# Kernel tuning notes

Measured on AMD Instinct MI355X. Metric: run time of the kernel, lower is better.

## Reference

```python
import jax, jax.numpy as jnp
import numpy as np

B, N, C = 32, 2048, 64  # graphs, points per graph, hidden channels


def _linear_params(key, fin, fout):
    k1, k2 = jax.random.split(key)
    bound = 1.0 / np.sqrt(fin)
    W = jax.random.uniform(k1, (fin, fout), minval=-bound, maxval=bound, dtype=jnp.float32)
    b = jax.random.uniform(k2, (fout,), minval=-bound, maxval=bound, dtype=jnp.float32)
    return W, b


def setup_inputs() -> dict:
    key = jax.random.key(0)
    ks = jax.random.split(key, 10)
    W1a, b1a = _linear_params(ks[0], 3 * 2 + 3, C)   # conv1 mlp layer 1 (h is pos, 3-dim)
    W1b, b1b = _linear_params(ks[1], C, C)
    W2a, b2a = _linear_params(ks[2], C * 2 + 3, C)   # conv2
    W2b, b2b = _linear_params(ks[3], C, C)
    W3a, b3a = _linear_params(ks[4], C * 2 + 3, C)   # conv3
    W3b, b3b = _linear_params(ks[5], C, C)
    Wr, br = _linear_params(ks[6], C, 6)
    pos = jax.random.normal(ks[7], (B * N, 3), dtype=jnp.float32)
    x = jax.random.normal(ks[8], (B * N, 3), dtype=jnp.float32)  # unused by forward (h=pos)
    batch = jnp.repeat(jnp.arange(B, dtype=jnp.int32), N)
    return dict(x=x, pos=pos, batch=batch,
                W1a=W1a, b1a=b1a, W1b=W1b, b1b=b1b,
                W2a=W2a, b2a=b2a, W2b=W2b, b2b=b2b,
                W3a=W3a, b3a=b3a, W3b=W3b, b3b=b3b,
                Wr=Wr, br=br)


_gather = jax.vmap(lambda a, i: a[i])  # per-graph fancy gather


def knn_idx(pos, k):
    # pos: [B, n, 3] -> idx [B, n, k] of k nearest neighbors (incl. self, loop=True)
    d2 = jnp.sum((pos[:, :, None, :] - pos[:, None, :, :]) ** 2, axis=-1)  # [B,n,n]
    _, idx = jax.lax.top_k(-d2, k)
    return idx


def fps_idx(pos_b, m):
    # farthest point sampling of m points from pos_b [n,3], deterministic start at 0
    d = jnp.sum((pos_b - pos_b[0]) ** 2, axis=-1)
    def body(d, _):
        i = jnp.argmax(d)
        d = jnp.minimum(d, jnp.sum((pos_b - pos_b[i]) ** 2, axis=-1))
        return d, i
    _, rest = jax.lax.scan(body, d, None, length=m - 1)
    return jnp.concatenate([jnp.zeros((1,), rest.dtype), rest])


def pointnet_layer(h, pos, idx, W1, b1, W2, b2):
    # h [B,n,Ch], pos [B,n,3], idx [B,n,k]; message = mlp(cat(h_i,h_j,pos_j-pos_i)); aggr = max
    h_j = _gather(h, idx)                      # [B,n,k,Ch]
    pos_j = _gather(pos, idx)                  # [B,n,k,3]
    rel = pos_j - pos[:, :, None, :]
    h_i = jnp.broadcast_to(h[:, :, None, :], h_j.shape)
    m = jnp.concatenate([h_i, h_j, rel], axis=-1)
    m = jax.nn.relu(m @ W1 + b1) @ W2 + b2
    return jnp.max(m, axis=2)                  # max over neighbors -> [B,n,C]


def reference(x, pos, batch,
              W1a, b1a, W1b, b1b,
              W2a, b2a, W2b, b2b,
              W3a, b3a, W3b, b3b,
              Wr, br):
    p = pos.reshape(B, N, 3)
    # layer 1: h = pos, k = 6
    h = jax.nn.relu(pointnet_layer(p, p, knn_idx(p, 6), W1a, b1a, W1b, b1b))
    # fps ratio 0.5 -> N/2
    sel = jax.vmap(lambda pb: fps_idx(pb, N // 2))(p)
    p, h = _gather(p, sel), _gather(h, sel)
    # layer 2: k = 4
    h = jax.nn.relu(pointnet_layer(h, p, knn_idx(p, 4), W2a, b2a, W2b, b2b))
    # fps -> N/4
    sel = jax.vmap(lambda pb: fps_idx(pb, N // 4))(p)
    p, h = _gather(p, sel), _gather(h, sel)
    # layer 3: k = 3
    h = jax.nn.relu(pointnet_layer(h, p, knn_idx(p, 3), W3a, b3a, W3b, b3b))
    g = jnp.max(h, axis=1)  # global max pool over points -> [B, C]
    return g @ Wr + br      # [B, 6]
```

## Files before the change

### kernel.cpp

```cpp
#include <hip/hip_runtime.h>
#include <hip/hip_bf16.h>
#include <math.h>

constexpr int B = 32;
constexpr int N = 2048;

__global__ void detect_kernel(const unsigned int* __restrict__ raw, int* __restrict__ flag) {
    __shared__ int cnt;
    if (threadIdx.x == 0) cnt = 0;
    __syncthreads();
    int c = 0;
    for (int i = threadIdx.x; i < 4096; i += 256) {
        unsigned h = (raw[i] >> 8) & 0x7f;
        if (h >= 0x3a && h <= 0x41) c++;
    }
    atomicAdd(&cnt, c);
    __syncthreads();
    if (threadIdx.x == 0) *flag = (cnt > (4096 * 55) / 100) ? 1 : 0;
}

__global__ void b2f_kernel(const void* __restrict__ in, float* __restrict__ out, int n,
                           const int* __restrict__ flag) {
    int i = blockIdx.x * 256 + threadIdx.x;
    if (i >= n) return;
    if (*flag) out[i] = __bfloat162float(((const __hip_bfloat16*)in)[i]);
    else       out[i] = ((const float*)in)[i];
}

struct B2FMulti {
    const void* src[14];
    float* dst[14];
    int n[14];
};

__global__ void b2f_multi_kernel(B2FMulti p, const int* __restrict__ flag) {
    int a = blockIdx.y;
    int i = blockIdx.x * 256 + threadIdx.x;
    if (i >= p.n[a]) return;
    if (*flag) p.dst[a][i] = __bfloat162float(((const __hip_bfloat16*)p.src[a])[i]);
    else       p.dst[a][i] = ((const float*)p.src[a])[i];
}

template <int K>
__global__ void __launch_bounds__(256) knn_kernel(const float* __restrict__ pos,
                                                  int* __restrict__ idx_out, int n) {
    #pragma clang fp contract(off)
    const int b = blockIdx.y;
    const int i = blockIdx.x * 256 + threadIdx.x;
    const float* pb = pos + (size_t)b * n * 3;
    const float xi = pb[i * 3 + 0], yi = pb[i * 3 + 1], zi = pb[i * 3 + 2];

    float bd[K];
    int   bi_[K];
    #pragma unroll
    for (int q = 0; q < K; ++q) { bd[q] = __builtin_inff(); bi_[q] = 0x7fffffff; }

    __shared__ float tx[256], ty[256], tz[256];
    for (int t0 = 0; t0 < n; t0 += 256) {
        __syncthreads();
        {
            int j = t0 + threadIdx.x;
            tx[threadIdx.x] = pb[j * 3 + 0];
            ty[threadIdx.x] = pb[j * 3 + 1];
            tz[threadIdx.x] = pb[j * 3 + 2];
        }
        __syncthreads();
        for (int jj = 0; jj < 256; ++jj) {
            float dx = xi - tx[jj], dy = yi - ty[jj], dz = zi - tz[jj];
            float d2 = (dx * dx + dy * dy) + dz * dz;
            int jg = t0 + jj;
            if (d2 < bd[K - 1] || (d2 == bd[K - 1] && jg < bi_[K - 1])) {
                bd[K - 1] = d2; bi_[K - 1] = jg;
                #pragma unroll
                for (int q = K - 1; q > 0; --q) {
                    bool sw = (bd[q] < bd[q - 1]) || (bd[q] == bd[q - 1] && bi_[q] < bi_[q - 1]);
                    if (sw) {
                        float td = bd[q]; bd[q] = bd[q - 1]; bd[q - 1] = td;
                        int   ti = bi_[q]; bi_[q] = bi_[q - 1]; bi_[q - 1] = ti;
                    }
                }
            }
        }
    }
    int* op = idx_out + ((size_t)b * n + i) * K;
    #pragma unroll
    for (int q = 0; q < K; ++q) op[q] = bi_[q];
}

template <int NPTS>
__device__ __forceinline__ void fps_phase(const float* __restrict__ px,
                                          const float* __restrict__ py,
                                          const float* __restrict__ pz,
                                          int* __restrict__ sel_lds,
                                          unsigned long long* __restrict__ slots,
                                          int m, int t) {
    #pragma clang fp contract(off)
    constexpr int P = NPTS / 256;
    float d[P], ox[P], oy[P], oz[P];
    unsigned int nk[P];
    const float sx = px[0], sy = py[0], sz = pz[0];
    #pragma unroll
    for (int p = 0; p < P; ++p) {
        const int ii = t * P + p;
        ox[p] = px[ii]; oy[p] = py[ii]; oz[p] = pz[ii];
        float dx = ox[p] - sx, dy = oy[p] - sy, dz = oz[p] - sz;
        d[p] = (dx * dx + dy * dy) + dz * dz;
        nk[p] = ~(unsigned)ii;
    }
    if (t == 0) sel_lds[0] = 0;

    for (int it = 1; it < m; ++it) {
        unsigned long long kb = ((unsigned long long)__float_as_uint(d[0]) << 32) | nk[0];
        #pragma unroll
        for (int p = 1; p < P; ++p) {
            unsigned long long key = ((unsigned long long)__float_as_uint(d[p]) << 32) | nk[p];
            if (key > kb) kb = key;
        }
        #pragma unroll
        for (int o = 1; o < 64; o <<= 1) {
            unsigned long long other = __shfl_xor(kb, o, 64);
            if (other > kb) kb = other;
        }
        if ((t & 63) == 0) slots[(it & 1) * 4 + (t >> 6)] = kb;
        __syncthreads();
        {
            const unsigned long long* sp = slots + (it & 1) * 4;
            unsigned long long k0 = sp[0], k1 = sp[1], k2 = sp[2], k3 = sp[3];
            if (k1 > k0) k0 = k1;
            if (k3 > k2) k2 = k3;
            kb = (k2 > k0) ? k2 : k0;
        }
        const int bix = (int)(~(unsigned)(kb & 0xffffffffULL));
        if (t == 0) sel_lds[it] = bix;
        const float nx = px[bix], ny = py[bix], nz = pz[bix];
        #pragma unroll
        for (int p = 0; p < P; ++p) {
            float dx = ox[p] - nx, dy = oy[p] - ny, dz = oz[p] - nz;
            float dd = (dx * dx + dy * dy) + dz * dz;
            d[p] = fminf(d[p], dd);
        }
    }
    __syncthreads();
}

__global__ void __launch_bounds__(256) mega_kernel(
        const float* __restrict__ posf, const int* __restrict__ idx1,
        const float* __restrict__ W1, const float* __restrict__ b1,
        const float* __restrict__ W2, const float* __restrict__ b2,
        float* __restrict__ h1, int* __restrict__ sel1, int* __restrict__ sel2,
        float* __restrict__ p2, float* __restrict__ p3) {
    __shared__ __align__(16) char smem[65536];
    const int t = threadIdx.x;

    if (blockIdx.x < B) {
        const int b = blockIdx.x;
        float* px = (float*)smem;
        float* py = px + 2048;
        float* pz = py + 2048;
        int*   sel1_l = (int*)(pz + 2048);
        float* qx = (float*)(sel1_l + 1024);
        float* qy = qx + 1024;
        float* qz = qy + 1024;
        int*   sel2_l = (int*)(qz + 1024);
        unsigned long long* slots = (unsigned long long*)(sel2_l + 512);

        const float* pb = posf + (size_t)b * N * 3;
        for (int i = t; i < N; i += 256) {
            px[i] = pb[i * 3 + 0]; py[i] = pb[i * 3 + 1]; pz[i] = pb[i * 3 + 2];
        }
        __syncthreads();

        fps_phase<2048>(px, py, pz, sel1_l, slots, 1024, t);

        for (int i = t; i < 1024; i += 256) {
            int s = sel1_l[i];
            qx[i] = px[s]; qy[i] = py[s]; qz[i] = pz[s];
            sel1[(size_t)b * 1024 + i] = s;
        }
        __syncthreads();
        for (int i = t; i < 1024; i += 256) {
            float* pp = p2 + ((size_t)b * 1024 + i) * 3;
            pp[0] = qx[i]; pp[1] = qy[i]; pp[2] = qz[i];
        }

        fps_phase<1024>(qx, qy, qz, sel2_l, slots, 512, t);

        for (int i = t; i < 512; i += 256) {
            int s = sel2_l[i];
            sel2[(size_t)b * 512 + i] = s;
            float* pp = p3 + ((size_t)b * 512 + i) * 3;
            pp[0] = qx[s]; pp[1] = qy[s]; pp[2] = qz[s];
        }
    } else {
        const int lane = t & 63, g = t >> 6;
        float* al = (float*)smem + g * 4096;
        const int flat = (blockIdx.x - B) * 256 + t;
        const int b = flat >> 11;
        const int i = flat & (N - 1);
        const float* pb = posf + (size_t)b * N * 3;
        const float xi = pb[i * 3 + 0], yi = pb[i * 3 + 1], zi = pb[i * 3 + 2];

        float acc[64];
        #pragma unroll
        for (int c = 0; c < 64; ++c) acc[c] = -__builtin_inff();

        const int* idxp = idx1 + (size_t)flat * 6;
        for (int kk = 0; kk < 6; ++kk) {
            const int j = idxp[kk];
            const float xj = pb[j * 3 + 0], yj = pb[j * 3 + 1], zj = pb[j * 3 + 2];
            const float mv[9] = {xi, yi, zi, xj, yj, zj, xj - xi, yj - yi, zj - zi};
            float a[64];
            #pragma unroll
            for (int e = 0; e < 64; ++e) a[e] = b1[e];
            #pragma unroll
            for (int d = 0; d < 9; ++d) {
                #pragma unroll
                for (int e = 0; e < 64; ++e) a[e] = fmaf(mv[d], W1[d * 64 + e], a[e]);
            }
            __syncthreads();
            #pragma unroll
            for (int e = 0; e < 64; ++e) al[e * 64 + lane] = fmaxf(a[e], 0.f);
            __syncthreads();
            float o[64];
            #pragma unroll
            for (int c = 0; c < 64; ++c) o[c] = b2[c];
            for (int e = 0; e < 64; ++e) {
                float av = al[e * 64 + lane];
                #pragma unroll
                for (int c = 0; c < 64; ++c) o[c] = fmaf(av, W2[e * 64 + c], o[c]);
            }
            #pragma unroll
            for (int c = 0; c < 64; ++c) acc[c] = fmaxf(acc[c], o[c]);
        }
        float* op = h1 + (size_t)flat * 64;
        #pragma unroll
        for (int c = 0; c < 64; ++c) op[c] = fmaxf(acc[c], 0.f);
    }
}

__global__ void gather_h_kernel(const float* __restrict__ h_in, const int* __restrict__ sel,
                                float* __restrict__ h_out, int n_in, int m) {
    const int b = blockIdx.y;
    const int tid = blockIdx.x * 256 + threadIdx.x;
    const int p = tid >> 6, c = tid & 63;
    if (p >= m) return;
    const int s = sel[(size_t)b * m + p];
    h_out[((size_t)b * m + p) * 64 + c] = h_in[((size_t)b * n_in + s) * 64 + c];
}

__global__ void __launch_bounds__(64) pointnet64_kernel(
        const float* __restrict__ h_in, const float* __restrict__ pos,
        const int* __restrict__ idx,
        const float* __restrict__ W1, const float* __restrict__ b1,
        const float* __restrict__ W2, const float* __restrict__ b2,
        float* __restrict__ out, int n, int k) {
    const int b = blockIdx.y, lane = threadIdx.x;
    const int i = blockIdx.x * 64 + lane;
    const float* pb = pos + (size_t)b * n * 3;
    const float* hb = h_in + (size_t)b * n * 64;
    const float xi = pb[i * 3 + 0], yi = pb[i * 3 + 1], zi = pb[i * 3 + 2];

    __shared__ float a_lds[64 * 64];

    float acc[64];
    #pragma unroll
    for (int c = 0; c < 64; ++c) acc[c] = -__builtin_inff();

    const int* idxp = idx + ((size_t)b * n + i) * k;
    const float* hi = hb + (size_t)i * 64;
    for (int kk = 0; kk < k; ++kk) {
        const int j = idxp[kk];
        const float xj = pb[j * 3 + 0], yj = pb[j * 3 + 1], zj = pb[j * 3 + 2];
        const float* hj = hb + (size_t)j * 64;

        float a[64];
        #pragma unroll
        for (int e = 0; e < 64; ++e) a[e] = b1[e];

        for (int d4 = 0; d4 < 16; ++d4) {
            float4 v = *(const float4*)(hi + d4 * 4);
            const float mu[4] = {v.x, v.y, v.z, v.w};
            const float* wr = W1 + (size_t)(d4 * 4) * 64;
            #pragma unroll
            for (int u = 0; u < 4; ++u) {
                #pragma unroll
                for (int e = 0; e < 64; ++e) a[e] = fmaf(mu[u], wr[u * 64 + e], a[e]);
            }
        }
        for (int d4 = 0; d4 < 16; ++d4) {
            float4 v = *(const float4*)(hj + d4 * 4);
            const float mu[4] = {v.x, v.y, v.z, v.w};
            const float* wr = W1 + (size_t)(64 + d4 * 4) * 64;
            #pragma unroll
            for (int u = 0; u < 4; ++u) {
                #pragma unroll
                for (int e = 0; e < 64; ++e) a[e] = fmaf(mu[u], wr[u * 64 + e], a[e]);
            }
        }
        {
            const float mr[3] = {xj - xi, yj - yi, zj - zi};
            #pragma unroll
            for (int d = 0; d < 3; ++d) {
                #pragma unroll
                for (int e = 0; e < 64; ++e) a[e] = fmaf(mr[d], W1[(128 + d) * 64 + e], a[e]);
            }
        }
        __syncthreads();
        #pragma unroll
        for (int e = 0; e < 64; ++e) a_lds[e * 64 + lane] = fmaxf(a[e], 0.f);
        __syncthreads();
        float o[64];
        #pragma unroll
        for (int c = 0; c < 64; ++c) o[c] = b2[c];
        for (int e = 0; e < 64; ++e) {
            float av = a_lds[e * 64 + lane];
            #pragma unroll
            for (int c = 0; c < 64; ++c) o[c] = fmaf(av, W2[e * 64 + c], o[c]);
        }
        #pragma unroll
        for (int c = 0; c < 64; ++c) acc[c] = fmaxf(acc[c], o[c]);
    }
    float* op = out + ((size_t)b * n + i) * 64;
    #pragma unroll
    for (int c = 0; c < 64; ++c) op[c] = fmaxf(acc[c], 0.f);
}

__global__ void __launch_bounds__(64) head_kernel(const float* __restrict__ h,
                                                  const float* __restrict__ Wr,
                                                  const float* __restrict__ br,
                                                  void* __restrict__ out, int n,
                                                  const int* __restrict__ flag) {
    const int b = blockIdx.x, lane = threadIdx.x;
    const float* hb = h + (size_t)b * n * 64;
    float g = -__builtin_inff();
    for (int i = 0; i < n; ++i) g = fmaxf(g, hb[(size_t)i * 64 + lane]);
    __shared__ float gl[64];
    gl[lane] = g;
    __syncthreads();
    if (lane < 6) {
        float o = br[lane];
        #pragma unroll
        for (int c = 0; c < 64; ++c) o = fmaf(gl[c], Wr[c * 6 + lane], o);
        if (*flag) ((__hip_bfloat16*)out)[b * 6 + lane] = __float2bfloat16(o);
        else       ((float*)out)[b * 6 + lane] = o;
    }
}

extern "C" void kernel_launch(void* const* d_in, const int* in_sizes, int n_in,
                              void* d_out, int out_size, void* d_ws, size_t ws_size,
                              hipStream_t stream) {
    (void)in_sizes; (void)n_in; (void)out_size; (void)ws_size;

    char* w = (char*)d_ws;
    auto alloc = [&](size_t nbytes) -> void* {
        void* p = (void*)w;
        w += (nbytes + 255) & ~(size_t)255;
        return p;
    };

    int*   flag = (int*)alloc(4);
    float* posf = (float*)alloc((size_t)B * N * 3 * 4);
    float* W1a = (float*)alloc(9 * 64 * 4);    float* b1a = (float*)alloc(64 * 4);
    float* W1b = (float*)alloc(64 * 64 * 4);   float* b1b = (float*)alloc(64 * 4);
    float* W2a = (float*)alloc(131 * 64 * 4);  float* b2a = (float*)alloc(64 * 4);
    float* W2b = (float*)alloc(64 * 64 * 4);   float* b2b = (float*)alloc(64 * 4);
    float* W3a = (float*)alloc(131 * 64 * 4);  float* b3a = (float*)alloc(64 * 4);
    float* W3b = (float*)alloc(64 * 64 * 4);   float* b3b = (float*)alloc(64 * 4);
    float* Wr  = (float*)alloc(64 * 6 * 4);    float* br  = (float*)alloc(6 * 4);

    float* h1    = (float*)alloc((size_t)B * N * 64 * 4);
    int*   idx1  = (int*)alloc((size_t)B * N * 6 * 4);
    int*   sel1  = (int*)alloc((size_t)B * 1024 * 4);
    float* p2    = (float*)alloc((size_t)B * 1024 * 3 * 4);
    float* h2in  = (float*)alloc((size_t)B * 1024 * 64 * 4);
    int*   idx2  = (int*)alloc((size_t)B * 1024 * 4 * 4);
    int*   sel2  = (int*)alloc((size_t)B * 512 * 4);
    float* p3    = (float*)alloc((size_t)B * 512 * 3 * 4);
    int*   idx3  = (int*)alloc((size_t)B * 512 * 3 * 4);
    float* h2out = h1;
    float* h3in  = h1 + (size_t)B * 1024 * 64;
    float* h3out = h1 + (size_t)B * 1024 * 64 + (size_t)B * 512 * 64;

    detect_kernel<<<dim3(1), 256, 0, stream>>>((const unsigned int*)d_in[1], flag);
    b2f_kernel<<<dim3((B * N * 3 + 255) / 256), 256, 0, stream>>>(d_in[1], posf, B * N * 3, flag);
    B2FMulti mp;
    {
        const int   wi[14] = {3, 4, 5, 6, 7, 8, 9, 10, 11, 12, 13, 14, 15, 16};
        float*      wd[14] = {W1a, b1a, W1b, b1b, W2a, b2a, W2b, b2b, W3a, b3a, W3b, b3b, Wr, br};
        const int   wn[14] = {576, 64, 4096, 64, 8384, 64, 4096, 64, 8384, 64, 4096, 64, 384, 6};
        for (int q = 0; q < 14; ++q) { mp.src[q] = d_in[wi[q]]; mp.dst[q] = wd[q]; mp.n[q] = wn[q]; }
    }
    b2f_multi_kernel<<<dim3(33, 14), 256, 0, stream>>>(mp, flag);

    knn_kernel<6><<<dim3(N / 256, B), 256, 0, stream>>>(posf, idx1, N);

    mega_kernel<<<dim3(B + (B * N) / 256), 256, 0, stream>>>(posf, idx1, W1a, b1a, W1b, b1b,
                                                             h1, sel1, sel2, p2, p3);

    gather_h_kernel<<<dim3(1024 * 64 / 256, B), 256, 0, stream>>>(h1, sel1, h2in, N, 1024);
    knn_kernel<4><<<dim3(1024 / 256, B), 256, 0, stream>>>(p2, idx2, 1024);
    pointnet64_kernel<<<dim3(1024 / 64, B), 64, 0, stream>>>(h2in, p2, idx2, W2a, b2a, W2b, b2b,
                                                             h2out, 1024, 4);

    gather_h_kernel<<<dim3(512 * 64 / 256, B), 256, 0, stream>>>(h2out, sel2, h3in, 1024, 512);
    knn_kernel<3><<<dim3(512 / 256, B), 256, 0, stream>>>(p3, idx3, 512);
    pointnet64_kernel<<<dim3(512 / 64, B), 64, 0, stream>>>(h3in, p3, idx3, W3a, b3a, W3b, b3b,
                                                            h3out, 512, 3);

    head_kernel<<<dim3(B), 64, 0, stream>>>(h3out, Wr, br, d_out, 512, flag);
}
```

Baseline: 2.276 ms.

## Fuse knn, gather and head into layer kernels; use DPP float argmax in FPS

Merges the two conversion kernels into one launch. The knn search now runs inside each layer kernel with the point coordinates staged in LDS, and the FPS gathers are folded into the layer-2 and layer-3 loads. The global max pool and regression head move into the layer-3 kernel using LDS atomics. FPS replaces the 64-bit shuffle argmax with a float DPP max, a ballot and a readlane. The kernels also drop the LDS-staged second MLP in favour of an all-register two-half loop. The aim is fewer launches and less intermediate global traffic. The cost is much higher register pressure, and layer 3 now runs on only 32 blocks of 512 threads, which lowers parallelism.

```diff
diff --git a/kernel.cpp b/kernel.cpp
--- a/kernel.cpp
+++ b/kernel.cpp
@@ -19,73 +19,20 @@
     if (threadIdx.x == 0) *flag = (cnt > (4096 * 55) / 100) ? 1 : 0;
 }
 
-__global__ void b2f_kernel(const void* __restrict__ in, float* __restrict__ out, int n,
-                           const int* __restrict__ flag) {
+struct ConvSeg { const void* src; float* dst; int n; };
+struct ConvParams { ConvSeg s[15]; };
+
+__global__ void convert_kernel(ConvParams p, const int* __restrict__ flag) {
+    const ConvSeg sg = p.s[blockIdx.y];
     int i = blockIdx.x * 256 + threadIdx.x;
-    if (i >= n) return;
-    if (*flag) out[i] = __bfloat162float(((const __hip_bfloat16*)in)[i]);
-    else       out[i] = ((const float*)in)[i];
-}
-
-struct B2FMulti {
-    const void* src[14];
-    float* dst[14];
-    int n[14];
-};
-
-__global__ void b2f_multi_kernel(B2FMulti p, const int* __restrict__ flag) {
-    int a = blockIdx.y;
-    int i = blockIdx.x * 256 + threadIdx.x;
-    if (i >= p.n[a]) return;
-    if (*flag) p.dst[a][i] = __bfloat162float(((const __hip_bfloat16*)p.src[a])[i]);
-    else       p.dst[a][i] = ((const float*)p.src[a])[i];
-}
-
-template <int K>
-__global__ void __launch_bounds__(256) knn_kernel(const float* __restrict__ pos,
-                                                  int* __restrict__ idx_out, int n) {
-    #pragma clang fp contract(off)
-    const int b = blockIdx.y;
-    const int i = blockIdx.x * 256 + threadIdx.x;
-    const float* pb = pos + (size_t)b * n * 3;
-    const float xi = pb[i * 3 + 0], yi = pb[i * 3 + 1], zi = pb[i * 3 + 2];
-
-    float bd[K];
-    int   bi_[K];
-    #pragma unroll
-    for (int q = 0; q < K; ++q) { bd[q] = __builtin_inff(); bi_[q] = 0x7fffffff; }
-
-    __shared__ float tx[256], ty[256], tz[256];
-    for (int t0 = 0; t0 < n; t0 += 256) {
-        __syncthreads();
-        {
-            int j = t0 + threadIdx.x;
-            tx[threadIdx.x] = pb[j * 3 + 0];
-            ty[threadIdx.x] = pb[j * 3 + 1];
-            tz[threadIdx.x] = pb[j * 3 + 2];
-        }
-        __syncthreads();
-        for (int jj = 0; jj < 256; ++jj) {
-            float dx = xi - tx[jj], dy = yi - ty[jj], dz = zi - tz[jj];
-            float d2 = (dx * dx + dy * dy) + dz * dz;
-            int jg = t0 + jj;
-            if (d2 < bd[K - 1] || (d2 == bd[K - 1] && jg < bi_[K - 1])) {
-                bd[K - 1] = d2; bi_[K - 1] = jg;
-                #pragma unroll
-                for (int q = K - 1; q > 0; --q) {
-                    bool sw = (bd[q] < bd[q - 1]) || (bd[q] == bd[q - 1] && bi_[q] < bi_[q - 1]);
-                    if (sw) {
-                        float td = bd[q]; bd[q] = bd[q - 1]; bd[q - 1] = td;
-                        int   ti = bi_[q]; bi_[q] = bi_[q - 1]; bi_[q - 1] = ti;
-                    }
-                }
-            }
-        }
-    }
-    int* op = idx_out + ((size_t)b * n + i) * K;
-    #pragma unroll
-    for (int q = 0; q < K; ++q) op[q] = bi_[q];
-}
+    if (i >= sg.n) return;
+    if (*flag) sg.dst[i] = __bfloat162float(((const __hip_bfloat16*)sg.src)[i]);
+    else       sg.dst[i] = ((const float*)sg.src)[i];
+}
+
+#define DPP_MAXF(v, ctrl)                                                      \
+    (v) = fmaxf((v), __int_as_float(__builtin_amdgcn_update_dpp(               \
+        __float_as_int(v), __float_as_int(v), (ctrl), 0xf, 0xf, false)))
 
 template <int NPTS>
 __device__ __forceinline__ void fps_phase(const float* __restrict__ px,
@@ -97,62 +44,145 @@
     #pragma clang fp contract(off)
     constexpr int P = NPTS / 256;
     float d[P], ox[P], oy[P], oz[P];
-    unsigned int nk[P];
-    const float sx = px[0], sy = py[0], sz = pz[0];
     #pragma unroll
     for (int p = 0; p < P; ++p) {
         const int ii = t * P + p;
         ox[p] = px[ii]; oy[p] = py[ii]; oz[p] = pz[ii];
-        float dx = ox[p] - sx, dy = oy[p] - sy, dz = oz[p] - sz;
-        d[p] = (dx * dx + dy * dy) + dz * dz;
-        nk[p] = ~(unsigned)ii;
+        d[p] = __builtin_inff();
     }
     if (t == 0) sel_lds[0] = 0;
+    float nx = px[0], ny = py[0], nz = pz[0];
 
     for (int it = 1; it < m; ++it) {
-        unsigned long long kb = ((unsigned long long)__float_as_uint(d[0]) << 32) | nk[0];
-        #pragma unroll
-        for (int p = 1; p < P; ++p) {
-            unsigned long long key = ((unsigned long long)__float_as_uint(d[p]) << 32) | nk[p];
-            if (key > kb) kb = key;
-        }
-        #pragma unroll
-        for (int o = 1; o < 64; o <<= 1) {
-            unsigned long long other = __shfl_xor(kb, o, 64);
-            if (other > kb) kb = other;
-        }
-        if ((t & 63) == 0) slots[(it & 1) * 4 + (t >> 6)] = kb;
-        __syncthreads();
-        {
-            const unsigned long long* sp = slots + (it & 1) * 4;
-            unsigned long long k0 = sp[0], k1 = sp[1], k2 = sp[2], k3 = sp[3];
-            if (k1 > k0) k0 = k1;
-            if (k3 > k2) k2 = k3;
-            kb = (k2 > k0) ? k2 : k0;
-        }
-        const int bix = (int)(~(unsigned)(kb & 0xffffffffULL));
-        if (t == 0) sel_lds[it] = bix;
-        const float nx = px[bix], ny = py[bix], nz = pz[bix];
+        float bv = -1.0f; int bix = 0;
         #pragma unroll
         for (int p = 0; p < P; ++p) {
             float dx = ox[p] - nx, dy = oy[p] - ny, dz = oz[p] - nz;
             float dd = (dx * dx + dy * dy) + dz * dz;
-            d[p] = fminf(d[p], dd);
-        }
-    }
-    __syncthreads();
-}
-
-__global__ void __launch_bounds__(256) mega_kernel(
-        const float* __restrict__ posf, const int* __restrict__ idx1,
+            float dn = fminf(d[p], dd);
+            d[p] = dn;
+            if (dn > bv) { bv = dn; bix = t * P + p; }
+        }
+        float r = bv;
+        DPP_MAXF(r, 0x111); DPP_MAXF(r, 0x112); DPP_MAXF(r, 0x114);
+        DPP_MAXF(r, 0x118); DPP_MAXF(r, 0x142); DPP_MAXF(r, 0x143);
+        const float gmax = __int_as_float(__builtin_amdgcn_readlane(__float_as_int(r), 63));
+        const unsigned long long msk = __ballot(bv == gmax);
+        const int wl = (int)__builtin_ctzll(msk);
+        const int widx = __builtin_amdgcn_readlane(bix, wl);
+        if ((t & 63) == 0) {
+            slots[(it & 1) * 4 + (t >> 6)] =
+                ((unsigned long long)(unsigned)__float_as_int(gmax) << 32) |
+                (unsigned)(~widx);
+        }
+        __syncthreads();
+        const unsigned long long* sp = slots + (it & 1) * 4;
+        unsigned long long k0 = sp[0], k1 = sp[1], k2 = sp[2], k3 = sp[3];
+        if (k1 > k0) k0 = k1;
+        if (k3 > k2) k2 = k3;
+        if (k2 > k0) k0 = k2;
+        const int g = ~(int)(unsigned)(k0 & 0xffffffffULL);
+        if (t == 0) sel_lds[it] = g;
+        nx = px[g]; ny = py[g]; nz = pz[g];
+    }
+    __syncthreads();
+}
+
+template <int K>
+__device__ __forceinline__ void knn_lds(const float* __restrict__ cx,
+                                        const float* __restrict__ cy,
+                                        const float* __restrict__ cz,
+                                        int n, float xi, float yi, float zi,
+                                        int* __restrict__ nb_l, int t, int tstride) {
+    #pragma clang fp contract(off)
+    float bd[K]; int bi_[K];
+    #pragma unroll
+    for (int q = 0; q < K; ++q) { bd[q] = __builtin_inff(); bi_[q] = 0x7fffffff; }
+    for (int j = 0; j < n; ++j) {
+        float dx = xi - cx[j], dy = yi - cy[j], dz = zi - cz[j];
+        float d2 = (dx * dx + dy * dy) + dz * dz;
+        if (d2 < bd[K - 1] || (d2 == bd[K - 1] && j < bi_[K - 1])) {
+            bd[K - 1] = d2; bi_[K - 1] = j;
+            #pragma unroll
+            for (int q = K - 1; q > 0; --q) {
+                bool sw = (bd[q] < bd[q - 1]) || (bd[q] == bd[q - 1] && bi_[q] < bi_[q - 1]);
+                if (sw) {
+                    float td = bd[q]; bd[q] = bd[q - 1]; bd[q - 1] = td;
+                    int   ti = bi_[q]; bi_[q] = bi_[q - 1]; bi_[q - 1] = ti;
+                }
+            }
+        }
+    }
+    #pragma unroll
+    for (int q = 0; q < K; ++q) nb_l[t + tstride * q] = bi_[q];
+}
+
+__device__ __forceinline__ void mlp131_acc(const float* __restrict__ hi,
+                                           const float* __restrict__ hj,
+                                           float rx, float ry, float rz,
+                                           const float* __restrict__ W1,
+                                           const float* __restrict__ b1,
+                                           const float* __restrict__ W2,
+                                           const float* __restrict__ b2,
+                                           float acc[64]) {
+    float a[64];
+    #pragma unroll
+    for (int e = 0; e < 64; ++e) a[e] = b1[e];
+    for (int d4 = 0; d4 < 16; ++d4) {
+        float4 v = *(const float4*)(hi + d4 * 4);
+        const float mu[4] = {v.x, v.y, v.z, v.w};
+        const float* wr = W1 + (size_t)(d4 * 4) * 64;
+        #pragma unroll
+        for (int u = 0; u < 4; ++u) {
+            #pragma unroll
+            for (int e = 0; e < 64; ++e) a[e] = fmaf(mu[u], wr[u * 64 + e], a[e]);
+        }
+    }
+    for (int d4 = 0; d4 < 16; ++d4) {
+        float4 v = *(const float4*)(hj + d4 * 4);
+        const float mu[4] = {v.x, v.y, v.z, v.w};
+        const float* wr = W1 + (size_t)(64 + d4 * 4) * 64;
+        #pragma unroll
+        for (int u = 0; u < 4; ++u) {
+            #pragma unroll
+            for (int e = 0; e < 64; ++e) a[e] = fmaf(mu[u], wr[u * 64 + e], a[e]);
+        }
+    }
+    {
+        const float mr[3] = {rx, ry, rz};
+        #pragma unroll
+        for (int d = 0; d < 3; ++d) {
+            #pragma unroll
+            for (int e = 0; e < 64; ++e) a[e] = fmaf(mr[d], W1[(128 + d) * 64 + e], a[e]);
+        }
+    }
+    #pragma unroll
+    for (int h = 0; h < 2; ++h) {
+        float o[32];
+        #pragma unroll
+        for (int c = 0; c < 32; ++c) o[c] = b2[h * 32 + c];
+        #pragma unroll
+        for (int e = 0; e < 64; ++e) {
+            float av = fmaxf(a[e], 0.f);
+            #pragma unroll
+            for (int c = 0; c < 32; ++c) o[c] = fmaf(av, W2[e * 64 + h * 32 + c], o[c]);
+        }
+        #pragma unroll
+        for (int c = 0; c < 32; ++c) acc[h * 32 + c] = fmaxf(acc[h * 32 + c], o[c]);
+    }
+}
+
+__global__ void __launch_bounds__(256) front_kernel(
+        const float* __restrict__ posf,
         const float* __restrict__ W1, const float* __restrict__ b1,
         const float* __restrict__ W2, const float* __restrict__ b2,
         float* __restrict__ h1, int* __restrict__ sel1, int* __restrict__ sel2,
         float* __restrict__ p2, float* __restrict__ p3) {
-    __shared__ __align__(16) char smem[65536];
+    __shared__ __align__(16) char smem[43136];
     const int t = threadIdx.x;
 
     if (blockIdx.x < B) {
+        __builtin_amdgcn_s_setprio(1);
         const int b = blockIdx.x;
         float* px = (float*)smem;
         float* py = px + 2048;
@@ -192,22 +222,29 @@
             pp[0] = qx[s]; pp[1] = qy[s]; pp[2] = qz[s];
         }
     } else {
-        const int lane = t & 63, g = t >> 6;
-        float* al = (float*)smem + g * 4096;
-        const int flat = (blockIdx.x - B) * 256 + t;
-        const int b = flat >> 11;
-        const int i = flat & (N - 1);
+        const int f = (int)blockIdx.x - B;
+        const int b = f >> 3;
+        const int i = ((f & 7) << 8) + t;
+        float* cx = (float*)smem;
+        float* cy = cx + 2048;
+        float* cz = cy + 2048;
+        int*   nb_l = (int*)(cz + 2048);
+
         const float* pb = posf + (size_t)b * N * 3;
-        const float xi = pb[i * 3 + 0], yi = pb[i * 3 + 1], zi = pb[i * 3 + 2];
+        for (int j = t; j < N; j += 256) {
+            cx[j] = pb[j * 3 + 0]; cy[j] = pb[j * 3 + 1]; cz[j] = pb[j * 3 + 2];
+        }
+        __syncthreads();
+        const float xi = cx[i], yi = cy[i], zi = cz[i];
+        knn_lds<6>(cx, cy, cz, N, xi, yi, zi, nb_l, t, 256);
 
         float acc[64];
         #pragma unroll
         for (int c = 0; c < 64; ++c) acc[c] = -__builtin_inff();
 
-        const int* idxp = idx1 + (size_t)flat * 6;
         for (int kk = 0; kk < 6; ++kk) {
-            const int j = idxp[kk];
-            const float xj = pb[j * 3 + 0], yj = pb[j * 3 + 1], zj = pb[j * 3 + 2];
+            const int j = nb_l[t + 256 * kk];
+            const float xj = cx[j], yj = cy[j], zj = cz[j];
             const float mv[9] = {xi, yi, zi, xj, yj, zj, xj - xi, yj - yi, zj - zi};
             float a[64];
             #pragma unroll
@@ -217,132 +254,109 @@
                 #pragma unroll
                 for (int e = 0; e < 64; ++e) a[e] = fmaf(mv[d], W1[d * 64 + e], a[e]);
             }
-            __syncthreads();
-            #pragma unroll
-            for (int e = 0; e < 64; ++e) al[e * 64 + lane] = fmaxf(a[e], 0.f);
-            __syncthreads();
-            float o[64];
-            #pragma unroll
-            for (int c = 0; c < 64; ++c) o[c] = b2[c];
-            for (int e = 0; e < 64; ++e) {
-                float av = al[e * 64 + lane];
+            #pragma unroll
+            for (int h = 0; h < 2; ++h) {
+                float o[32];
                 #pragma unroll
-                for (int c = 0; c < 64; ++c) o[c] = fmaf(av, W2[e * 64 + c], o[c]);
+                for (int c = 0; c < 32; ++c) o[c] = b2[h * 32 + c];
+                #pragma unroll
+                for (int e = 0; e < 64; ++e) {
+                    float av = fmaxf(a[e], 0.f);
+                    #pragma unroll
+                    for (int c = 0; c < 32; ++c) o[c] = fmaf(av, W2[e * 64 + h * 32 + c], o[c]);
+                }
+                #pragma unroll
+                for (int c = 0; c < 32; ++c) acc[h * 32 + c] = fmaxf(acc[h * 32 + c], o[c]);
             }
-            #pragma unroll
-            for (int c = 0; c < 64; ++c) acc[c] = fmaxf(acc[c], o[c]);
-        }
-        float* op = h1 + (size_t)flat * 64;
+        }
+        float* op = h1 + ((size_t)b * N + i) * 64;
         #pragma unroll
         for (int c = 0; c < 64; ++c) op[c] = fmaxf(acc[c], 0.f);
     }
 }
 
-__global__ void gather_h_kernel(const float* __restrict__ h_in, const int* __restrict__ sel,
-                                float* __restrict__ h_out, int n_in, int m) {
-    const int b = blockIdx.y;
-    const int tid = blockIdx.x * 256 + threadIdx.x;
-    const int p = tid >> 6, c = tid & 63;
-    if (p >= m) return;
-    const int s = sel[(size_t)b * m + p];
-    h_out[((size_t)b * m + p) * 64 + c] = h_in[((size_t)b * n_in + s) * 64 + c];
-}
-
-__global__ void __launch_bounds__(64) pointnet64_kernel(
-        const float* __restrict__ h_in, const float* __restrict__ pos,
-        const int* __restrict__ idx,
+__global__ void __launch_bounds__(256) layer2_kernel(
+        const float* __restrict__ h1, const float* __restrict__ p2,
+        const int* __restrict__ sel1,
         const float* __restrict__ W1, const float* __restrict__ b1,
         const float* __restrict__ W2, const float* __restrict__ b2,
-        float* __restrict__ out, int n, int k) {
-    const int b = blockIdx.y, lane = threadIdx.x;
-    const int i = blockIdx.x * 64 + lane;
-    const float* pb = pos + (size_t)b * n * 3;
-    const float* hb = h_in + (size_t)b * n * 64;
-    const float xi = pb[i * 3 + 0], yi = pb[i * 3 + 1], zi = pb[i * 3 + 2];
-
-    __shared__ float a_lds[64 * 64];
+        float* __restrict__ h2out) {
+    __shared__ float qx[1024], qy[1024], qz[1024];
+    __shared__ int nb_l[256 * 4];
+    const int t = threadIdx.x;
+    const int b = blockIdx.x >> 2;
+    const int i = ((blockIdx.x & 3) << 8) + t;
+
+    const float* pb = p2 + (size_t)b * 1024 * 3;
+    for (int j = t; j < 1024; j += 256) {
+        qx[j] = pb[j * 3 + 0]; qy[j] = pb[j * 3 + 1]; qz[j] = pb[j * 3 + 2];
+    }
+    __syncthreads();
+    const float xi = qx[i], yi = qy[i], zi = qz[i];
+    knn_lds<4>(qx, qy, qz, 1024, xi, yi, zi, nb_l, t, 256);
+
+    const int s1i = sel1[(size_t)b * 1024 + i];
+    const float* hi = h1 + ((size_t)b * N + s1i) * 64;
 
     float acc[64];
     #pragma unroll
     for (int c = 0; c < 64; ++c) acc[c] = -__builtin_inff();
 
-    const int* idxp = idx + ((size_t)b * n + i) * k;
-    const float* hi = hb + (size_t)i * 64;
-    for (int kk = 0; kk < k; ++kk) {
-        const int j = idxp[kk];
-        const float xj = pb[j * 3 + 0], yj = pb[j * 3 + 1], zj = pb[j * 3 + 2];
-        const float* hj = hb + (size_t)j * 64;
-
-        float a[64];
-        #pragma unroll
-        for (int e = 0; e < 64; ++e) a[e] = b1[e];
-
-        for (int d4 = 0; d4 < 16; ++d4) {
-            float4 v = *(const float4*)(hi + d4 * 4);
-            const float mu[4] = {v.x, v.y, v.z, v.w};
-            const float* wr = W1 + (size_t)(d4 * 4) * 64;
-            #pragma unroll
-            for (int u = 0; u < 4; ++u) {
-                #pragma unroll
-                for (int e = 0; e < 64; ++e) a[e] = fmaf(mu[u], wr[u * 64 + e], a[e]);
-            }
-        }
-        for (int d4 = 0; d4 < 16; ++d4) {
-            float4 v = *(const float4*)(hj + d4 * 4);
-            const float mu[4] = {v.x, v.y, v.z, v.w};
-            const float* wr = W1 + (size_t)(64 + d4 * 4) * 64;
-            #pragma unroll
-            for (int u = 0; u < 4; ++u) {
-                #pragma unroll
-                for (int e = 0; e < 64; ++e) a[e] = fmaf(mu[u], wr[u * 64 + e], a[e]);
-            }
-        }
-        {
-            const float mr[3] = {xj - xi, yj - yi, zj - zi};
-            #pragma unroll
-            for (int d = 0; d < 3; ++d) {
-                #pragma unroll
-                for (int e = 0; e < 64; ++e) a[e] = fmaf(mr[d], W1[(128 + d) * 64 + e], a[e]);
-            }
-        }
-        __syncthreads();
-        #pragma unroll
-        for (int e = 0; e < 64; ++e) a_lds[e * 64 + lane] = fmaxf(a[e], 0.f);
-        __syncthreads();
-        float o[64];
-        #pragma unroll
-        for (int c = 0; c < 64; ++c) o[c] = b2[c];
-        for (int e = 0; e < 64; ++e) {
-            float av = a_lds[e * 64 + lane];
-            #pragma unroll
-            for (int c = 0; c < 64; ++c) o[c] = fmaf(av, W2[e * 64 + c], o[c]);
-        }
-        #pragma unroll
-        for (int c = 0; c < 64; ++c) acc[c] = fmaxf(acc[c], o[c]);
-    }
-    float* op = out + ((size_t)b * n + i) * 64;
+    for (int kk = 0; kk < 4; ++kk) {
+        const int j = nb_l[t + 256 * kk];
+        const int s1j = sel1[(size_t)b * 1024 + j];
+        const float* hj = h1 + ((size_t)b * N + s1j) * 64;
+        mlp131_acc(hi, hj, qx[j] - xi, qy[j] - yi, qz[j] - zi, W1, b1, W2, b2, acc);
+    }
+    float* op = h2out + ((size_t)b * 1024 + i) * 64;
     #pragma unroll
     for (int c = 0; c < 64; ++c) op[c] = fmaxf(acc[c], 0.f);
 }
 
-__global__ void __launch_bounds__(64) head_kernel(const float* __restrict__ h,
-                                                  const float* __restrict__ Wr,
-                                                  const float* __restrict__ br,
-                                                  void* __restrict__ out, int n,
-                                                  const int* __restrict__ flag) {
-    const int b = blockIdx.x, lane = threadIdx.x;
-    const float* hb = h + (size_t)b * n * 64;
-    float g = -__builtin_inff();
-    for (int i = 0; i < n; ++i) g = fmaxf(g, hb[(size_t)i * 64 + lane]);
-    __shared__ float gl[64];
-    gl[lane] = g;
-    __syncthreads();
-    if (lane < 6) {
-        float o = br[lane];
-        #pragma unroll
-        for (int c = 0; c < 64; ++c) o = fmaf(gl[c], Wr[c * 6 + lane], o);
-        if (*flag) ((__hip_bfloat16*)out)[b * 6 + lane] = __float2bfloat16(o);
-        else       ((float*)out)[b * 6 + lane] = o;
+__global__ void __launch_bounds__(512) layer3_kernel(
+        const float* __restrict__ h2, const float* __restrict__ p3,
+        const int* __restrict__ sel2,
+        const float* __restrict__ W1, const float* __restrict__ b1,
+        const float* __restrict__ W2, const float* __restrict__ b2,
+        const float* __restrict__ Wr, const float* __restrict__ br,
+        void* __restrict__ out, const int* __restrict__ flag) {
+    __shared__ float qx[512], qy[512], qz[512];
+    __shared__ int nb_l[512 * 3];
+    __shared__ int gbits[64];
+    const int t = threadIdx.x;
+    const int b = blockIdx.x;
+
+    const float* pb = p3 + (size_t)b * 512 * 3;
+    if (t < 512) { qx[t] = pb[t * 3 + 0]; qy[t] = pb[t * 3 + 1]; qz[t] = pb[t * 3 + 2]; }
+    if (t < 64) gbits[t] = 0;
+    __syncthreads();
+    const float xi = qx[t], yi = qy[t], zi = qz[t];
+    knn_lds<3>(qx, qy, qz, 512, xi, yi, zi, nb_l, t, 512);
+
+    const int s2i = sel2[(size_t)b * 512 + t];
+    const float* hi = h2 + ((size_t)b * 1024 + s2i) * 64;
+
+    float acc[64];
+    #pragma unroll
+    for (int c = 0; c < 64; ++c) acc[c] = -__builtin_inff();
+
+    for (int kk = 0; kk < 3; ++kk) {
+        const int j = nb_l[t + 512 * kk];
+        const int s2j = sel2[(size_t)b * 512 + j];
+        const float* hj = h2 + ((size_t)b * 1024 + s2j) * 64;
+        mlp131_acc(hi, hj, qx[j] - xi, qy[j] - yi, qz[j] - zi, W1, b1, W2, b2, acc);
+    }
+    #pragma unroll
+    for (int c = 0; c < 64; ++c) {
+        atomicMax(&gbits[c], __float_as_int(fmaxf(acc[c], 0.f)));
+    }
+    __syncthreads();
+    if (t < 6) {
+        float o = br[t];
+        #pragma unroll
+        for (int c = 0; c < 64; ++c) o = fmaf(__int_as_float(gbits[c]), Wr[c * 6 + t], o);
+        if (*flag) ((__hip_bfloat16*)out)[b * 6 + t] = __float2bfloat16(o);
+        else       ((float*)out)[b * 6 + t] = o;
     }
 }
 
@@ -369,43 +383,27 @@
     float* Wr  = (float*)alloc(64 * 6 * 4);    float* br  = (float*)alloc(6 * 4);
 
     float* h1    = (float*)alloc((size_t)B * N * 64 * 4);
-    int*   idx1  = (int*)alloc((size_t)B * N * 6 * 4);
+    float* h2out = (float*)alloc((size_t)B * 1024 * 64 * 4);
     int*   sel1  = (int*)alloc((size_t)B * 1024 * 4);
+    int*   sel2  = (int*)alloc((size_t)B * 512 * 4);
     float* p2    = (float*)alloc((size_t)B * 1024 * 3 * 4);
-    float* h2in  = (float*)alloc((size_t)B * 1024 * 64 * 4);
-    int*   idx2  = (int*)alloc((size_t)B * 1024 * 4 * 4);
-    int*   sel2  = (int*)alloc((size_t)B * 512 * 4);
     float* p3    = (float*)alloc((size_t)B * 512 * 3 * 4);
-    int*   idx3  = (int*)alloc((size_t)B * 512 * 3 * 4);
-    float* h2out = h1;
-    float* h3in  = h1 + (size_t)B * 1024 * 64;
-    float* h3out = h1 + (size_t)B * 1024 * 64 + (size_t)B * 512 * 64;
 
     detect_kernel<<<dim3(1), 256, 0, stream>>>((const unsigned int*)d_in[1], flag);
-    b2f_kernel<<<dim3((B * N * 3 + 255) / 256), 256, 0, stream>>>(d_in[1], posf, B * N * 3, flag);
-    B2FMulti mp;
+    ConvParams cp;
     {
-        const int   wi[14] = {3, 4, 5, 6, 7, 8, 9, 10, 11, 12, 13, 14, 15, 16};
-        float*      wd[14] = {W1a, b1a, W1b, b1b, W2a, b2a, W2b, b2b, W3a, b3a, W3b, b3b, Wr, br};
-        const int   wn[14] = {576, 64, 4096, 64, 8384, 64, 4096, 64, 8384, 64, 4096, 64, 384, 6};
-        for (int q = 0; q < 14; ++q) { mp.src[q] = d_in[wi[q]]; mp.dst[q] = wd[q]; mp.n[q] = wn[q]; }
-    }
-    b2f_multi_kernel<<<dim3(33, 14), 256, 0, stream>>>(mp, flag);
-
-    knn_kernel<6><<<dim3(N / 256, B), 256, 0, stream>>>(posf, idx1, N);
-
-    mega_kernel<<<dim3(B + (B * N) / 256), 256, 0, stream>>>(posf, idx1, W1a, b1a, W1b, b1b,
-                                                             h1, sel1, sel2, p2, p3);
-
-    gather_h_kernel<<<dim3(1024 * 64 / 256, B), 256, 0, stream>>>(h1, sel1, h2in, N, 1024);
-    knn_kernel<4><<<dim3(1024 / 256, B), 256, 0, stream>>>(p2, idx2, 1024);
-    pointnet64_kernel<<<dim3(1024 / 64, B), 64, 0, stream>>>(h2in, p2, idx2, W2a, b2a, W2b, b2b,
-                                                             h2out, 1024, 4);
-
-    gather_h_kernel<<<dim3(512 * 64 / 256, B), 256, 0, stream>>>(h2out, sel2, h3in, 1024, 512);
-    knn_kernel<3><<<dim3(512 / 256, B), 256, 0, stream>>>(p3, idx3, 512);
-    pointnet64_kernel<<<dim3(512 / 64, B), 64, 0, stream>>>(h3in, p3, idx3, W3a, b3a, W3b, b3b,
-                                                            h3out, 512, 3);
-
-    head_kernel<<<dim3(B), 64, 0, stream>>>(h3out, Wr, br, d_out, 512, flag);
-}
+        float* wd[15] = {posf, W1a, b1a, W1b, b1b, W2a, b2a, W2b, b2b, W3a, b3a, W3b, b3b, Wr, br};
+        const int wi[15] = {1, 3, 4, 5, 6, 7, 8, 9, 10, 11, 12, 13, 14, 15, 16};
+        const int wn[15] = {B * N * 3, 576, 64, 4096, 64, 8384, 64, 4096, 64, 8384, 64, 4096, 64, 384, 6};
+        for (int q = 0; q < 15; ++q) { cp.s[q].src = d_in[wi[q]]; cp.s[q].dst = wd[q]; cp.s[q].n = wn[q]; }
+    }
+    convert_kernel<<<dim3((B * N * 3 + 255) / 256, 15), 256, 0, stream>>>(cp, flag);
+
+    front_kernel<<<dim3(B + 256), 256, 0, stream>>>(posf, W1a, b1a, W1b, b1b,
+                                                    h1, sel1, sel2, p2, p3);
+
+    layer2_kernel<<<dim3(128), 256, 0, stream>>>(h1, p2, sel1, W2a, b2a, W2b, b2b, h2out);
+
+    layer3_kernel<<<dim3(B), 512, 0, stream>>>(h2out, p3, sel2, W3a, b3a, W3b, b3b,
+                                               Wr, br, d_out, flag);
+}
```

Result: slower. 2.643 ms (+16.1%).
